# Kernel tuning notes

Hardware: AMD Instinct MI355X
Metric: run time of the kernel (lower is better)

## Reference

```python
import jax, jax.numpy as jnp
import numpy as np

HEADS = 16
HEAD_DIM = 64
DIM = 1024
INNER = HEADS * HEAD_DIM  # 1024


def setup_inputs() -> dict:
    key = jax.random.key(0)
    k1, k2, k3, k4 = jax.random.split(key, 4)
    B, S = 4, 2048
    x = jax.random.normal(k1, (B, S, DIM), dtype=jnp.float32)
    # Dense(inner*3, use_bias=False): kernel [dim, 3*inner]
    w_qkv = jax.random.normal(k2, (DIM, 3 * INNER), dtype=jnp.float32) * (DIM ** -0.5)
    # to_out: Dense(dim) with bias (Dropout(0.0) is identity at inference)
    w_out = jax.random.normal(k3, (INNER, DIM), dtype=jnp.float32) * (INNER ** -0.5)
    b_out = jax.random.normal(k4, (DIM,), dtype=jnp.float32) * 0.02
    return {"x": x, "w_qkv": w_qkv, "w_out": w_out, "b_out": b_out}


def reference(x, w_qkv, w_out, b_out):
    B, S, _ = x.shape
    scale = HEAD_DIM ** -0.5
    qkv = x @ w_qkv                                   # [B,S,3*inner]
    q, k, v = jnp.split(qkv, 3, axis=-1)              # each [B,S,inner]
    def to_heads(t):
        return jnp.transpose(t.reshape(B, S, HEADS, HEAD_DIM), (0, 2, 1, 3))  # [B,H,S,D]
    q, k, v = to_heads(q), to_heads(k), to_heads(v)
    dots = jnp.einsum("bhid,bhjd->bhij", q, k) * scale  # [B,H,S,S]
    attn = jax.nn.softmax(dots, axis=-1)
    out = jnp.einsum("bhij,bhjd->bhid", attn, v)        # [B,H,S,D]
    # Faithful to original: reshape [B,H,S,D] -> [B,S,H*D] WITHOUT transposing heads back.
    out = out.reshape(B, S, HEADS * HEAD_DIM)
    return out @ w_out + b_out
```

## Files before the change

### kernel.cpp

```cpp
#include <hip/hip_runtime.h>
#include <hip/hip_bf16.h>
#include <stdint.h>

typedef __bf16 bf16;
typedef __bf16 bf16x4 __attribute__((ext_vector_type(4)));
typedef __bf16 bf16x8 __attribute__((ext_vector_type(8)));
typedef float  f32x4  __attribute__((ext_vector_type(4)));

#define MFMA16(a, b, c) __builtin_amdgcn_mfma_f32_16x16x32_bf16((a), (b), (c), 0, 0, 0)
#define EXP2(x) __builtin_amdgcn_exp2f(x)

__device__ __forceinline__ void gload_lds16(const void* g, void* l) {
  __builtin_amdgcn_global_load_lds((const __attribute__((address_space(1))) void*)g,
                                   (__attribute__((address_space(3))) void*)l,
                                   16, 0, 0);
}


__global__ __launch_bounds__(256) void k_cast(const float4* __restrict__ in,
                                              bf16x4* __restrict__ out, int n4) {
  int i = blockIdx.x * 256 + threadIdx.x;
  if (i < n4) {
    float4 v = in[i];
    bf16x4 o = {(bf16)v.x, (bf16)v.y, (bf16)v.z, (bf16)v.w};
    out[i] = o;
  }
}

__global__ __launch_bounds__(256) void k_transpose(const float* __restrict__ in,
                                                   bf16* __restrict__ out,
                                                   int K, int N) {
  __shared__ float tile[32][33];
  int n0 = blockIdx.x * 32, k0 = blockIdx.y * 32;
  int tx = threadIdx.x, ty = threadIdx.y;
#pragma unroll
  for (int i = 0; i < 4; ++i)
    tile[ty + i * 8][tx] = in[(size_t)(k0 + ty + i * 8) * N + n0 + tx];
  __syncthreads();
#pragma unroll
  for (int i = 0; i < 4; ++i)
    out[(size_t)(n0 + ty + i * 8) * K + k0 + tx] = (bf16)tile[tx][ty + i * 8];
}


template <typename Epi>
__device__ __forceinline__ void gemm128(const bf16* __restrict__ A,
                                        const bf16* __restrict__ Bt, Epi epi) {
  __shared__ alignas(16) bf16 As[128][32];
  __shared__ alignas(16) bf16 Bs[128][32];
  const int tid = threadIdx.x;
  const int lane = tid & 63, wv = tid >> 6;
  const int l16 = lane & 15, q4 = lane >> 4;
  const int bm = blockIdx.x * 128, bn = blockIdx.y * 128;
  const int wm = (wv >> 1) * 64, wn = (wv & 1) * 64;

  const f32x4 Z4 = {0.f, 0.f, 0.f, 0.f};
  f32x4 acc[4][4];
#pragma unroll
  for (int mi = 0; mi < 4; ++mi)
#pragma unroll
    for (int ni = 0; ni < 4; ++ni) acc[mi][ni] = Z4;

  const int srow = wv * 32 + (lane >> 2);
  const int scol = (lane & 3) * 8;
  const bf16* ga = A + (size_t)(bm + srow) * 1024 + scol;
  const bf16* gb = Bt + (size_t)(bn + srow) * 1024 + scol;

  for (int k0 = 0; k0 < 1024; k0 += 32) {
    __syncthreads();
#pragma unroll
    for (int c = 0; c < 2; ++c) {
      gload_lds16(ga + (size_t)c * 16 * 1024 + k0, &As[wv * 32 + c * 16][0]);
      gload_lds16(gb + (size_t)c * 16 * 1024 + k0, &Bs[wv * 32 + c * 16][0]);
    }
    __syncthreads();

    bf16x8 af[4], bfr[4];
#pragma unroll
    for (int i = 0; i < 4; ++i) {
      af[i]  = *(const bf16x8*)&As[wm + i * 16 + l16][q4 * 8];
      bfr[i] = *(const bf16x8*)&Bs[wn + i * 16 + l16][q4 * 8];
    }
#pragma unroll
    for (int mi = 0; mi < 4; ++mi)
#pragma unroll
      for (int ni = 0; ni < 4; ++ni)
        acc[mi][ni] = MFMA16(af[mi], bfr[ni], acc[mi][ni]);
  }

#pragma unroll
  for (int mi = 0; mi < 4; ++mi)
#pragma unroll
    for (int ni = 0; ni < 4; ++ni) {
      int m0 = bm + wm + mi * 16 + q4 * 4;
      int n  = bn + wn + ni * 16 + l16;
      epi(m0, n, acc[mi][ni]);
    }
}

#define QSCALE (0.125f * 1.44269504088896f)

__global__ __launch_bounds__(256) void k_gemm_qkv(const bf16* __restrict__ xb,
                                                  const bf16* __restrict__ wt,
                                                  bf16* __restrict__ Q,
                                                  bf16* __restrict__ Kd,
                                                  bf16* __restrict__ Vt) {
  gemm128(xb, wt, [=](int m0, int n, f32x4 v) {
    int b = m0 >> 11, s0 = m0 & 2047;
    int sect = n >> 10, nn = n & 1023;
    int h = nn >> 6, d = nn & 63;
    size_t bh = (size_t)b * 16 + h;
    if (sect == 0) {
#pragma unroll
      for (int r = 0; r < 4; ++r)
        Q[(bh * 2048 + s0 + r) * 64 + d] = (bf16)(v[r] * QSCALE);
    } else if (sect == 1) {
#pragma unroll
      for (int r = 0; r < 4; ++r)
        Kd[(bh * 2048 + s0 + r) * 64 + d] = (bf16)v[r];
    } else {
      bf16x4 pk = {(bf16)v[0], (bf16)v[1], (bf16)v[2], (bf16)v[3]};
      *(bf16x4*)(Vt + (bh * 64 + d) * 2048 + s0) = pk;
    }
  });
}

__global__ __launch_bounds__(256) void k_gemm_out(const bf16* __restrict__ o2,
                                                  const bf16* __restrict__ wt,
                                                  const float* __restrict__ bias,
                                                  float* __restrict__ out) {
  gemm128(o2, wt, [=](int m0, int n, f32x4 v) {
    float bn = bias[n];
#pragma unroll
    for (int r = 0; r < 4; ++r)
      out[(size_t)(m0 + r) * 1024 + n] = v[r] + bn;
  });
}


#define STAGE_KV(KT, BUF)                                                        \
  do {                                                                           \
    const int _kt = (KT);                                                        \
    _Pragma("unroll") for (int r = 0; r < 2; ++r) {                              \
      int i = r * 256 + tid;                  \
      int row = i >> 3, sl = i & 7;                                              \
      int gsl = sl ^ (row & 7);                                                  \
      gload_lds16(Kbase + (size_t)(_kt * 64 + row) * 64 + gsl * 8,               \
                  (bf16*)&Ks[BUF][0][0] + (size_t)(r * 256 + wv * 64) * 8);      \
      gload_lds16(Vbase + (size_t)row * 2048 + _kt * 64 + gsl * 8,               \
                  (bf16*)&Vs[BUF][0][0] + (size_t)(r * 256 + wv * 64) * 8);      \
    }                                                                            \
  } while (0)

__global__ __launch_bounds__(256, 3) void k_attn(const bf16* __restrict__ Q,
                                                 const bf16* __restrict__ Kd,
                                                 const bf16* __restrict__ Vt,
                                                 bf16* __restrict__ out2) {
  __shared__ alignas(16) bf16 Ks[2][64][64];
  __shared__ alignas(16) bf16 Vs[2][64][64];
  __shared__ alignas(16) bf16 P_lds[4][32][64];
  const int tid = threadIdx.x, lane = tid & 63, wv = tid >> 6;
  const int l16 = lane & 15, q4 = lane >> 4;
  const int bh = blockIdx.y;
  const int b = bh >> 4, h = bh & 15;
  const int q0 = blockIdx.x * 128 + wv * 32;

  const bf16* Kbase = Kd + (size_t)bh * 2048 * 64;
  const bf16* Vbase = Vt + (size_t)bh * 64 * 2048;

  bf16x8 qf[2][2];
#pragma unroll
  for (int mf = 0; mf < 2; ++mf)
#pragma unroll
    for (int kk = 0; kk < 2; ++kk)
      qf[mf][kk] = *(const bf16x8*)(Q + ((size_t)bh * 2048 + q0 + mf * 16 + l16) * 64 +
                                    kk * 32 + q4 * 8);

  const f32x4 Z4 = {0.f, 0.f, 0.f, 0.f};
  float m_r[2], l_r[2];
  f32x4 acc_o[2][4];
#pragma unroll
  for (int mf = 0; mf < 2; ++mf) {
    m_r[mf] = -__builtin_inff();
    l_r[mf] = 0.f;
#pragma unroll
    for (int df = 0; df < 4; ++df) acc_o[mf][df] = Z4;
  }

  STAGE_KV(0, 0);
  __syncthreads();

  for (int kt = 0; kt < 32; ++kt) {
    const int cur = kt & 1;
    STAGE_KV(kt + 1 <= 31 ? kt + 1 : 31, cur ^ 1);

    bf16x8 kf[2][4], vfr[2][4];
#pragma unroll
    for (int kk = 0; kk < 2; ++kk)
#pragma unroll
      for (int nf = 0; nf < 4; ++nf)
        kf[kk][nf] = *(const bf16x8*)&Ks[cur][nf * 16 + l16][((kk * 4 + q4) ^ (l16 & 7)) * 8];
#pragma unroll
    for (int kk = 0; kk < 2; ++kk)
#pragma unroll
      for (int df = 0; df < 4; ++df)
        vfr[kk][df] = *(const bf16x8*)&Vs[cur][df * 16 + l16][((kk * 4 + q4) ^ (l16 & 7)) * 8];

    f32x4 s_acc[2][4];
#pragma unroll
    for (int mf = 0; mf < 2; ++mf)
#pragma unroll
      for (int nf = 0; nf < 4; ++nf) s_acc[mf][nf] = Z4;
    __builtin_amdgcn_s_setprio(1);
#pragma unroll
    for (int kk = 0; kk < 2; ++kk)
#pragma unroll
      for (int nf = 0; nf < 4; ++nf)
#pragma unroll
        for (int mf = 0; mf < 2; ++mf)
          s_acc[mf][nf] = MFMA16(kf[kk][nf], qf[mf][kk], s_acc[mf][nf]);
    __builtin_amdgcn_s_setprio(0);

    float fmf[2];
#pragma unroll
    for (int mf = 0; mf < 2; ++mf) {
      float t = s_acc[mf][0][0];
#pragma unroll
      for (int nf = 0; nf < 4; ++nf)
#pragma unroll
        for (int r = 0; r < 4; ++r)
          if (nf | r) t = fmaxf(t, s_acc[mf][nf][r]);
      t = fmaxf(t, __shfl_xor(t, 16));
      t = fmaxf(t, __shfl_xor(t, 32));
      float mn = fmaxf(m_r[mf], t);
      float f = EXP2(m_r[mf] - mn);
      float ps = 0.f;
      const int row = mf * 16 + l16;
#pragma unroll
      for (int nf = 0; nf < 4; ++nf) {
        float pv0 = EXP2(s_acc[mf][nf][0] - mn);
        float pv1 = EXP2(s_acc[mf][nf][1] - mn);
        float pv2 = EXP2(s_acc[mf][nf][2] - mn);
        float pv3 = EXP2(s_acc[mf][nf][3] - mn);
        ps += (pv0 + pv1) + (pv2 + pv3);
        bf16x4 pk = {(bf16)pv0, (bf16)pv1, (bf16)pv2, (bf16)pv3};
        int slot = (nf * 4 + q4) ^ (l16 & 14);
        *(bf16x4*)&P_lds[wv][row][slot * 4] = pk;
      }
      ps += __shfl_xor(ps, 16);
      ps += __shfl_xor(ps, 32);
      l_r[mf] = l_r[mf] * f + ps;
      m_r[mf] = mn;
      fmf[mf] = f;
    }
#pragma unroll
    for (int mf = 0; mf < 2; ++mf)
#pragma unroll
      for (int df = 0; df < 4; ++df) acc_o[mf][df] *= fmf[mf];

#pragma unroll
    for (int kk2 = 0; kk2 < 2; ++kk2) {
      bf16x8 pf[2];
#pragma unroll
      for (int mf = 0; mf < 2; ++mf) {
        int row = mf * 16 + l16;
        int pbase = ((kk2 * 8 + q4 * 2) ^ (l16 & 14)) * 4;
        pf[mf] = *(const bf16x8*)&P_lds[wv][row][pbase];
      }
      __builtin_amdgcn_s_setprio(1);
#pragma unroll
      for (int df = 0; df < 4; ++df)
#pragma unroll
        for (int mf = 0; mf < 2; ++mf)
          acc_o[mf][df] = MFMA16(vfr[kk2][df], pf[mf], acc_o[mf][df]);
      __builtin_amdgcn_s_setprio(0);
    }

    __syncthreads();
  }

#pragma unroll
  for (int mf = 0; mf < 2; ++mf) {
    float inv = 1.0f / l_r[mf];
    int s = q0 + mf * 16 + l16;
    int row2 = h * 128 + (s >> 4);
    size_t base = ((size_t)b * 2048 + row2) * 1024 + (s & 15) * 64;
#pragma unroll
    for (int df = 0; df < 4; ++df)
#pragma unroll
      for (int r = 0; r < 4; ++r) {
        int d = df * 16 + q4 * 4 + r;
        out2[base + d] = (bf16)(acc_o[mf][df][r] * inv);
      }
  }
}


extern "C" void kernel_launch(void* const* d_in, const int* in_sizes, int n_in,
                              void* d_out, int out_size, void* d_ws, size_t ws_size,
                              hipStream_t stream) {
  const float* x     = (const float*)d_in[0];
  const float* w_qkv = (const float*)d_in[1];
  const float* w_out = (const float*)d_in[2];
  const float* b_out = (const float*)d_in[3];
  float* out = (float*)d_out;

  char* ws = (char*)d_ws;
  size_t off = 0;
  auto alloc = [&](size_t bytes) {
    void* p = ws + off;
    off += (bytes + 255) & ~(size_t)255;
    return p;
  };
  bf16* xb    = (bf16*)alloc((size_t)8192 * 1024 * 2);
  bf16* wqkvT = (bf16*)alloc((size_t)3072 * 1024 * 2);
  bf16* woutT = (bf16*)alloc((size_t)1024 * 1024 * 2);
  bf16* Q     = (bf16*)alloc((size_t)64 * 2048 * 64 * 2);
  bf16* Kd    = (bf16*)alloc((size_t)64 * 2048 * 64 * 2);
  bf16* Vt    = (bf16*)alloc((size_t)64 * 64 * 2048 * 2);
  bf16* out2  = xb;

  k_cast<<<8192, 256, 0, stream>>>((const float4*)x, (bf16x4*)xb, 8192 * 1024 / 4);
  k_transpose<<<dim3(96, 32), dim3(32, 8), 0, stream>>>(w_qkv, wqkvT, 1024, 3072);
  k_transpose<<<dim3(32, 32), dim3(32, 8), 0, stream>>>(w_out, woutT, 1024, 1024);
  k_gemm_qkv<<<dim3(64, 24), 256, 0, stream>>>(xb, wqkvT, Q, Kd, Vt);
  k_attn<<<dim3(16, 64), 256, 0, stream>>>(Q, Kd, Vt, out2);
  k_gemm_out<<<dim3(64, 8), 256, 0, stream>>>(out2, woutT, b_out, out);
}
```

Before: 298.8 us.

## Double-buffer GEMM LDS tiles with XOR swizzle and MFMA priority boost

Adds a second LDS buffer to the shared 128x128 GEMM so the global-to-LDS loads for the next K-step are issued before the current step's MFMAs, leaving one barrier per iteration. The LDS layout is XOR-swizzled by row so the per-lane fragment reads spread across banks. It also raises wave priority around the MFMA block. The cost is double the LDS per block, which may lower occupancy. There is also a risk that the async loads are not waited on before the barrier.

```diff
diff --git a/kernel.cpp b/kernel.cpp
--- a/kernel.cpp
+++ b/kernel.cpp
@@ -43,17 +43,33 @@
 }
 
 
+#define GEMM_STAGE(K0, BUF)                                                \
+  do {                                                                     \
+    _Pragma("unroll") for (int c = 0; c < 2; ++c) {                        \
+      int i = c * 256 + tid;            \
+      int row = i >> 2, u = i & 3;                                         \
+      int gu = u ^ (row & 3);                                              \
+      gload_lds16(ga_base + (size_t)row * 1024 + (K0) + gu * 8,            \
+                  (bf16*)&As[BUF][0][0] + (size_t)i * 8);                  \
+      gload_lds16(gb_base + (size_t)row * 1024 + (K0) + gu * 8,            \
+                  (bf16*)&Bs[BUF][0][0] + (size_t)i * 8);                  \
+    }                                                                      \
+  } while (0)
+
 template <typename Epi>
 __device__ __forceinline__ void gemm128(const bf16* __restrict__ A,
                                         const bf16* __restrict__ Bt, Epi epi) {
-  __shared__ alignas(16) bf16 As[128][32];
-  __shared__ alignas(16) bf16 Bs[128][32];
+  __shared__ alignas(16) bf16 As[2][128][32];
+  __shared__ alignas(16) bf16 Bs[2][128][32];
   const int tid = threadIdx.x;
   const int lane = tid & 63, wv = tid >> 6;
   const int l16 = lane & 15, q4 = lane >> 4;
   const int bm = blockIdx.x * 128, bn = blockIdx.y * 128;
   const int wm = (wv >> 1) * 64, wn = (wv & 1) * 64;
 
+  const bf16* ga_base = A + (size_t)bm * 1024;
+  const bf16* gb_base = Bt + (size_t)bn * 1024;
+
   const f32x4 Z4 = {0.f, 0.f, 0.f, 0.f};
   f32x4 acc[4][4];
 #pragma unroll
@@ -61,31 +77,29 @@
 #pragma unroll
     for (int ni = 0; ni < 4; ++ni) acc[mi][ni] = Z4;
 
-  const int srow = wv * 32 + (lane >> 2);
-  const int scol = (lane & 3) * 8;
-  const bf16* ga = A + (size_t)(bm + srow) * 1024 + scol;
-  const bf16* gb = Bt + (size_t)(bn + srow) * 1024 + scol;
-
+  GEMM_STAGE(0, 0);
+  __syncthreads();
+
+  const int ru = (q4 ^ (l16 & 3)) * 8;
   for (int k0 = 0; k0 < 1024; k0 += 32) {
-    __syncthreads();
-#pragma unroll
-    for (int c = 0; c < 2; ++c) {
-      gload_lds16(ga + (size_t)c * 16 * 1024 + k0, &As[wv * 32 + c * 16][0]);
-      gload_lds16(gb + (size_t)c * 16 * 1024 + k0, &Bs[wv * 32 + c * 16][0]);
-    }
-    __syncthreads();
+    const int cur = (k0 >> 5) & 1;
+    if (k0 + 32 < 1024) GEMM_STAGE(k0 + 32, cur ^ 1);
 
     bf16x8 af[4], bfr[4];
 #pragma unroll
     for (int i = 0; i < 4; ++i) {
-      af[i]  = *(const bf16x8*)&As[wm + i * 16 + l16][q4 * 8];
-      bfr[i] = *(const bf16x8*)&Bs[wn + i * 16 + l16][q4 * 8];
-    }
+      af[i]  = *(const bf16x8*)&As[cur][wm + i * 16 + l16][ru];
+      bfr[i] = *(const bf16x8*)&Bs[cur][wn + i * 16 + l16][ru];
+    }
+    __builtin_amdgcn_s_setprio(1);
 #pragma unroll
     for (int mi = 0; mi < 4; ++mi)
 #pragma unroll
       for (int ni = 0; ni < 4; ++ni)
         acc[mi][ni] = MFMA16(af[mi], bfr[ni], acc[mi][ni]);
+    __builtin_amdgcn_s_setprio(0);
+
+    __syncthreads();
   }
 
 #pragma unroll
```

Measured after the change: 294.0 us. Within noise of the previous version (-1.6%).
